# Performance work log

Measured on AMD Instinct MI355X. Metric: run time of the kernel, lower is better.

## Reference

```python
import jax, jax.numpy as jnp
import numpy as np
from jax import lax

SEQ_LEN, BATCH, POSE, H, PRED_LEN = 32, 32768, 34, 16, 15


def setup_inputs() -> dict:
    key = jax.random.key(0)
    ks = jax.random.split(key, 22)
    w = lambda k, s: (jax.random.normal(k, s, jnp.float32) * 0.1)
    return {
        "obs_s": jax.random.normal(ks[0], (SEQ_LEN, BATCH, POSE), jnp.float32),
        "enc_Wih": w(ks[1], (4 * H, POSE)), "enc_Whh": w(ks[2], (4 * H, H)),
        "enc_bih": w(ks[3], (4 * H,)), "enc_bhh": w(ks[4], (4 * H,)),
        "dec_Wih": w(ks[5], (4 * H, POSE)), "dec_Whh": w(ks[6], (4 * H, H)),
        "dec_bih": w(ks[7], (4 * H,)), "dec_bhh": w(ks[8], (4 * H,)),
        "cr_Wih": w(ks[9], (4 * H, POSE)), "cr_Whh": w(ks[10], (4 * H, H)),
        "cr_bih": w(ks[11], (4 * H,)), "cr_bhh": w(ks[12], (4 * H,)),
        "fc_W": w(ks[13], (POSE, H)), "fc_b": w(ks[14], (POSE,)),
        "fcc_W": w(ks[15], (2, H)), "fcc_b": w(ks[16], (2,)),
        "mlp_W": w(ks[17], (H, H)), "mlp_b": w(ks[18], (H,)),
        "emb_W": w(ks[19], (POSE, 2)), "emb_b": w(ks[20], (POSE,)),
        "pred_len": PRED_LEN,
    }


def _cell(x, h, c, Wih, Whh, bih, bhh):
    # torch LSTM gate order: i, f, g, o
    gates = x @ Wih.T + bih + h @ Whh.T + bhh  # [B, 4H]
    i, f, g, o = jnp.split(gates, 4, axis=-1)
    c = jax.nn.sigmoid(f) * c + jax.nn.sigmoid(i) * jnp.tanh(g)
    h = jax.nn.sigmoid(o) * jnp.tanh(c)
    return h, c


def reference(obs_s, enc_Wih, enc_Whh, enc_bih, enc_bhh,
              dec_Wih, dec_Whh, dec_bih, dec_bhh,
              cr_Wih, cr_Whh, cr_bih, cr_bhh,
              fc_W, fc_b, fcc_W, fcc_b, mlp_W, mlp_b, emb_W, emb_b,
              pred_len):
    batch = obs_s.shape[1]
    h0 = jnp.zeros((batch, H), obs_s.dtype)
    c0 = jnp.zeros((batch, H), obs_s.dtype)

    def enc_step(carry, x):
        h, c = _cell(x, *carry, enc_Wih, enc_Whh, enc_bih, enc_bhh)
        return (h, c), None

    (h, c), _ = lax.scan(enc_step, (h0, c0), obs_s)

    hc = h @ mlp_W.T + mlp_b           # crossing hidden init from encoder h
    cc = jnp.zeros_like(hc)
    last_s = obs_s[-1]                 # [B, POSE]
    last_cr = obs_s[-1]

    def dec_step(carry, _):
        h, c, hc, cc, last_s, last_cr = carry
        hc, cc = _cell(last_cr, hc, cc, cr_Wih, cr_Whh, cr_bih, cr_bhh)
        curr_cr = jax.nn.softmax(hc @ fcc_W.T + fcc_b, axis=-1)   # [B, 2]
        next_cr = curr_cr @ emb_W.T + emb_b                        # [B, POSE]
        h, c = _cell(last_s, h, c, dec_Wih, dec_Whh, dec_bih, dec_bhh)
        curr_s = h @ fc_W.T + fc_b                                 # [B, POSE]
        return (h, c, hc, cc, curr_s, next_cr), (curr_s, curr_cr)

    _, (pred_s, pred_crossing) = lax.scan(
        dec_step, (h, c, hc, cc, last_s, last_cr), None, length=pred_len)
    return pred_s, pred_crossing
```

## Files before the change

kernel.cpp:

```cpp
#include <hip/hip_runtime.h>
#include <cstddef>

#define SEQLEN 32
#define BATCH  32768
#define POSE   34
#define PREDL  15
#define LOG2E  1.4426950408889634f
#define K2E    2.8853901817779268f

typedef __attribute__((ext_vector_type(8))) short short8;
typedef __attribute__((ext_vector_type(4))) float f32x4;
typedef union { short8 s8; unsigned u[4]; } pk8;

#define MF(a,b,c) __builtin_amdgcn_mfma_f32_16x16x32_bf16(a,b,c,0,0,0)
#define EXP2(x)  __builtin_amdgcn_exp2f(x)
#define RCP(x)   __builtin_amdgcn_rcpf(x)

__device__ __forceinline__ unsigned short f2bf(float f){ __bf16 b=(__bf16)f; return __builtin_bit_cast(unsigned short,b); }
__device__ __forceinline__ unsigned f22bf(float lo,float hi){ return (unsigned)f2bf(lo) | ((unsigned)f2bf(hi)<<16); }
__device__ __forceinline__ short8 zero8(){ pk8 r; r.u[0]=0;r.u[1]=0;r.u[2]=0;r.u[3]=0; return r.s8; }
__device__ __forceinline__ float scGT(int gt){ return (gt==2)?K2E:LOG2E; }

__device__ __forceinline__ short8 g8s(const float* __restrict__ p, float s){
    pk8 r;
    r.u[0]=f22bf(p[0]*s,p[1]*s); r.u[1]=f22bf(p[2]*s,p[3]*s);
    r.u[2]=f22bf(p[4]*s,p[5]*s); r.u[3]=f22bf(p[6]*s,p[7]*s);
    return r.s8;
}

__device__ __forceinline__ void pw4v(const f32x4 (&ac)[4], f32x4 &cs,
                                     unsigned &hp0, unsigned &hp1){
    f32x4 A,C,B,O;
#pragma unroll
    for(int j=0;j<4;++j){
        A[j]=EXP2(-ac[0][j]); C[j]=EXP2(-ac[1][j]);
        B[j]=EXP2( ac[2][j]); O[j]=EXP2(-ac[3][j]);
    }
    const f32x4 one={1.f,1.f,1.f,1.f};
    f32x4 u=one+A, w=one+C, v=B+one, Bm=B-one;
    f32x4 t1=u*v;
    f32x4 num=cs*t1+Bm*w;
    f32x4 den=t1*w;
    f32x4 rd_,E,rh;
#pragma unroll
    for(int j=0;j<4;++j) rd_[j]=RCP(den[j]);
    f32x4 cn=num*rd_;
    cs=cn;
#pragma unroll
    for(int j=0;j<4;++j) E[j]=EXP2(K2E*cn[j]);
    f32x4 hd=(one+O)*(E+one);
#pragma unroll
    for(int j=0;j<4;++j) rh[j]=RCP(hd[j]);
    f32x4 hv=(E-one)*rh;
    hp0=f22bf(hv[0],hv[1]); hp1=f22bf(hv[2],hv[3]);
}

extern "C" __global__ void __launch_bounds__(256,2) lstm_enc(
    const float* __restrict__ obs_s,
    const float* __restrict__ eWih, const float* __restrict__ eWhh,
    const float* __restrict__ ebih, const float* __restrict__ ebhh,
    const float* __restrict__ mlpW, const float* __restrict__ mlpb,
    const float* __restrict__ dWih, const float* __restrict__ dWhh,
    const float* __restrict__ dbih, const float* __restrict__ dbhh,
    const float* __restrict__ cWih, const float* __restrict__ cWhh,
    const float* __restrict__ cbih, const float* __restrict__ cbhh,
    const float* __restrict__ fcW,  const float* __restrict__ fcb,
    const float* __restrict__ embW, const float* __restrict__ embb,
    float* __restrict__ wsBD, float* __restrict__ wsBC,
    unsigned short* __restrict__ wsDh, unsigned short* __restrict__ wsCh,
    unsigned short* __restrict__ wsCp, unsigned* __restrict__ hand)
{
    __shared__ unsigned xt4[4][4][320];

    if(blockIdx.x>=512){
        for(int idx=threadIdx.x; idx<1024; idx+=256){
            int R=idx>>4, k=idx&15;
            float s=scGT(R>>4);
            float vD=dWhh[R*16+k];
            for(int p=0;p<34;++p) vD=fmaf(dWih[R*34+p],fcW[p*16+k],vD);
            wsDh[idx]=f2bf(vD*s);
            wsCh[idx]=f2bf(cWhh[R*16+k]*s);
        }
        for(int idx=threadIdx.x; idx<128; idx+=256){
            int R=idx>>1, k=idx&1;
            float s=scGT(R>>4);
            float v=0.f;
            for(int p=0;p<34;++p) v=fmaf(cWih[R*34+p],embW[2*p+k],v);
            wsCp[idx]=f2bf(v*s);
        }
        for(int idx=threadIdx.x; idx<64; idx+=256){
            int R=idx;
            float s=scGT(R>>4);
            float vD=dbih[R]+dbhh[R], vC=cbih[R]+cbhh[R];
            for(int p=0;p<34;++p){ vD=fmaf(dWih[R*34+p],fcb[p],vD); vC=fmaf(cWih[R*34+p],embb[p],vC); }
            wsBD[idx]=vD*s; wsBC[idx]=vC*s;
        }
        return;
    }

    const int tid=threadIdx.x;
    const int l=tid&63;
    const int wv=tid>>6;
    const int lo=l&15, g=l>>4;
    const int pb=blockIdx.x*64 + wv*16;
    unsigned* XT=&xt4[wv][0][0];

    unsigned pofs[5]; int wofs[5];
#pragma unroll
    for(int it=0; it<5; ++it){
        int i2=l+64*it;
        int r=i2/17, w=i2-r*17;
        pofs[it]=(unsigned)((pb+r)*17+w);
        wofs[it]=r*20+w;
    }

    short8 wEx[4], wEhT[4]; f32x4 biasE[4];
#pragma unroll
    for(int gt=0;gt<4;++gt){
        float s=scGT(gt);
        int R=gt*16+lo;
        wEx[gt]=g8s(&eWih[R*34+8*g], s);
        pk8 r2;
        r2.u[0]=f22bf(eWhh[R*16+4*g]*s,   eWhh[R*16+4*g+1]*s);
        r2.u[1]=f22bf(eWhh[R*16+4*g+2]*s, eWhh[R*16+4*g+3]*s);
        r2.u[2]=(g==0)? f22bf(eWih[R*34+32]*s, eWih[R*34+33]*s) : 0u;
        r2.u[3]=0u;
        wEhT[gt]=r2.s8;
        float4 ba=*(const float4*)&ebih[gt*16+4*g];
        float4 bb=*(const float4*)&ebhh[gt*16+4*g];
        biasE[gt]=f32x4{(ba.x+bb.x)*s,(ba.y+bb.y)*s,(ba.z+bb.z)*s,(ba.w+bb.w)*s};
    }

    f32x4 cS={0.f,0.f,0.f,0.f};
    unsigned hp0=0u, hp1=0u;

    float2 RA[4][5];
    auto ldblk=[&](int t0){
#pragma unroll
        for(int s=0;s<4;++s){
            const float2* base=(const float2*)obs_s + (size_t)(t0+s)*(BATCH*17);
#pragma unroll
            for(int it=0;it<5;++it)
                if(it<4 || l<16) RA[s][it]=base[pofs[it]];
        }
    };
    auto wrblk=[&](){
#pragma unroll
        for(int s=0;s<4;++s)
#pragma unroll
            for(int it=0;it<5;++it)
                if(it<4 || l<16) XT[s*320+wofs[it]]=f22bf(RA[s][it].x,RA[s][it].y);
    };

    ldblk(0);
#pragma unroll 1
    for(int kb=0;kb<8;++kb){
        wrblk();
        if(kb+1<8) ldblk(4*(kb+1));
        short8 bx[4]; unsigned tw[4];
#pragma unroll
        for(int s=0;s<4;++s){
            bx[s]=*(const short8*)&XT[s*320+lo*20+4*g];
            tw[s]=XT[s*320+lo*20+16];
        }
        f32x4 cx[4][4];
#pragma unroll
        for(int s=0;s<4;++s)
#pragma unroll
            for(int gt=0;gt<4;++gt)
                cx[s][gt]=MF(wEx[gt],bx[s],biasE[gt]);
#pragma unroll
        for(int s=0;s<4;++s){
            pk8 bh; bh.u[0]=hp0; bh.u[1]=hp1; bh.u[2]=(g==0)?tw[s]:0u; bh.u[3]=0u;
            f32x4 acc[4];
#pragma unroll
            for(int gt=0;gt<4;++gt) acc[gt]=MF(wEhT[gt],bh.s8,cx[s][gt]);
            pw4v(acc,cS,hp0,hp1);
        }
    }

    unsigned hcp0,hcp1;
    {
        pk8 r;
        r.u[0]=f22bf(mlpW[lo*16+4*g],   mlpW[lo*16+4*g+1]);
        r.u[1]=f22bf(mlpW[lo*16+4*g+2], mlpW[lo*16+4*g+3]);
        r.u[2]=0u; r.u[3]=0u;
        f32x4 mb=*(const f32x4*)&mlpb[4*g];
        pk8 bh; bh.u[0]=hp0; bh.u[1]=hp1; bh.u[2]=0u; bh.u[3]=0u;
        f32x4 o=MF(r.s8,bh.s8,mb);
        hcp0=f22bf(o[0],o[1]); hcp1=f22bf(o[2],o[3]);
    }

    unsigned* Hw = hand + ((size_t)(blockIdx.x*4+wv)*64 + l)*8;
    Hw[0]=hp0; Hw[1]=hp1; Hw[2]=hcp0; Hw[3]=hcp1;
    *(f32x4*)(Hw+4)=cS;
}

extern "C" __global__ void __launch_bounds__(256,2) lstm_dec(
    const float* __restrict__ obs_s,
    const float* __restrict__ dWih, const float* __restrict__ dWhh,
    const float* __restrict__ dbih, const float* __restrict__ dbhh,
    const float* __restrict__ cWih, const float* __restrict__ cWhh,
    const float* __restrict__ cbih, const float* __restrict__ cbhh,
    const float* __restrict__ fcW,  const float* __restrict__ fcb,
    const float* __restrict__ fccW, const float* __restrict__ fccb,
    const float* __restrict__ wsBD, const float* __restrict__ wsBC,
    const unsigned short* __restrict__ wsDh, const unsigned short* __restrict__ wsCh,
    const unsigned short* __restrict__ wsCp, const unsigned* __restrict__ hand,
    float* __restrict__ out_s, float* __restrict__ out_cr)
{
    const int tid=threadIdx.x;
    const int l=tid&63;
    const int wv=tid>>6;
    const int lo=l&15, g=l>>4;
    const int grp=blockIdx.x*2+(wv>>1);
    const int role=__builtin_amdgcn_readfirstlane(wv&1);
    const int pb=grp*16;

    const unsigned* H = hand + ((size_t)grp*64 + l)*8;
    unsigned h0w=H[0], h1w=H[1], hc0w=H[2], hc1w=H[3];
    f32x4 csIn=*(const f32x4*)(H+4);

    const float* px=obs_s+((size_t)(SEQLEN-1)*BATCH+pb+lo)*POSE;
    short8 fbQ;
    {
        const float2* p2=(const float2*)(px+8*g);
        float2 q0=p2[0],q1=p2[1],q2=p2[2],q3=p2[3];
        pk8 r;
        r.u[0]=f22bf(q0.x,q0.y); r.u[1]=f22bf(q1.x,q1.y);
        r.u[2]=f22bf(q2.x,q2.y); r.u[3]=f22bf(q3.x,q3.y);
        fbQ=r.s8;
    }
    unsigned ftQ=f22bf(px[32],px[33]);

    if(role==0){
        f32x4 cS=csIn;
        unsigned hp0=h0w, hp1=h1w;
        f32x4 aD[4];
        {
#pragma unroll
            for(int gt=0;gt<4;++gt){
                float s=scGT(gt);
                int R=gt*16+lo;
                short8 d1=g8s(&dWih[R*34+8*g], s);
                pk8 d2;
                d2.u[0]=f22bf(dWhh[R*16+4*g]*s,   dWhh[R*16+4*g+1]*s);
                d2.u[1]=f22bf(dWhh[R*16+4*g+2]*s, dWhh[R*16+4*g+3]*s);
                d2.u[2]=(g==0)? f22bf(dWih[R*34+32]*s, dWih[R*34+33]*s) : 0u;
                d2.u[3]=0u;
                float4 da=*(const float4*)&dbih[gt*16+4*g];
                float4 db=*(const float4*)&dbhh[gt*16+4*g];
                f32x4 bd0={(da.x+db.x)*s,(da.y+db.y)*s,(da.z+db.z)*s,(da.w+db.w)*s};
                pk8 bhd; bhd.u[0]=hp0; bhd.u[1]=hp1; bhd.u[2]=(g==0)?ftQ:0u; bhd.u[3]=0u;
                f32x4 dx=MF(d1,fbQ,bd0);
                aD[gt]=MF(d2.s8,bhd.s8,dx);
            }
        }
        short8 wF[3]; f32x4 fcbF[3];
#pragma unroll
        for(int nt=0;nt<3;++nt){
            int np=nt*16+lo;
            if(np<POSE){
                pk8 r;
                r.u[0]=f22bf(fcW[np*16+4*g],   fcW[np*16+4*g+1]);
                r.u[1]=f22bf(fcW[np*16+4*g+2], fcW[np*16+4*g+3]);
                r.u[2]=0u; r.u[3]=0u;
                wF[nt]=r.s8;
            } else wF[nt]=zero8();
#pragma unroll
            for(int j=0;j<4;++j){
                int row=nt*16+4*g+j;
                fcbF[nt][j]=(row<POSE)? fcb[row] : 0.f;
            }
        }
        short8 wDh[4]; f32x4 biasD[4];
#pragma unroll
        for(int gt=0;gt<4;++gt){
            int R=gt*16+lo;
            uint2 qd=*(const uint2*)&wsDh[R*16+4*g];
            pk8 rd; rd.u[0]=qd.x; rd.u[1]=qd.y; rd.u[2]=0u; rd.u[3]=0u;
            wDh[gt]=rd.s8;
            biasD[gt]=*(const f32x4*)&wsBD[gt*16+4*g];
        }
#pragma unroll 1
        for(int s=0;s<PREDL;++s){
            pw4v(aD,cS,hp0,hp1);
            pk8 bh; bh.u[0]=hp0; bh.u[1]=hp1; bh.u[2]=0u; bh.u[3]=0u;
            f32x4 o0=MF(wF[0],bh.s8,fcbF[0]);
            f32x4 o1=MF(wF[1],bh.s8,fcbF[1]);
            f32x4 o2=MF(wF[2],bh.s8,fcbF[2]);
            float* po = out_s + ((size_t)s*BATCH + pb + lo)*POSE;
            *(float2*)(po+4*g)     =make_float2(o0[0],o0[1]);
            *(float2*)(po+4*g+2)   =make_float2(o0[2],o0[3]);
            *(float2*)(po+16+4*g)  =make_float2(o1[0],o1[1]);
            *(float2*)(po+16+4*g+2)=make_float2(o1[2],o1[3]);
            if(g==0) *(float2*)(po+32)=make_float2(o2[0],o2[1]);
            if(s+1<PREDL){
#pragma unroll
                for(int gt=0;gt<4;++gt) aD[gt]=MF(wDh[gt],bh.s8,biasD[gt]);
            }
        }
    } else {
        f32x4 cC={0.f,0.f,0.f,0.f};
        unsigned hcp0=hc0w, hcp1=hc1w, pp=0u;
        f32x4 aC[4];
        {
#pragma unroll
            for(int gt=0;gt<4;++gt){
                float s=scGT(gt);
                int R=gt*16+lo;
                short8 a1=g8s(&cWih[R*34+8*g], s);
                pk8 a2;
                a2.u[0]=f22bf(cWhh[R*16+4*g]*s,   cWhh[R*16+4*g+1]*s);
                a2.u[1]=f22bf(cWhh[R*16+4*g+2]*s, cWhh[R*16+4*g+3]*s);
                a2.u[2]=(g==0)? f22bf(cWih[R*34+32]*s, cWih[R*34+33]*s) : 0u;
                a2.u[3]=0u;
                float4 ba=*(const float4*)&cbih[gt*16+4*g];
                float4 bb=*(const float4*)&cbhh[gt*16+4*g];
                f32x4 bc0={(ba.x+bb.x)*s,(ba.y+bb.y)*s,(ba.z+bb.z)*s,(ba.w+bb.w)*s};
                pk8 bhc; bhc.u[0]=hcp0; bhc.u[1]=hcp1; bhc.u[2]=(g==0)?ftQ:0u; bhc.u[3]=0u;
                f32x4 cx=MF(a1,fbQ,bc0);
                aC[gt]=MF(a2.s8,bhc.s8,cx);
            }
        }
        short8 wFC; f32x4 fccC;
        if(lo<2){
            pk8 r;
            r.u[0]=f22bf(fccW[lo*16+4*g],   fccW[lo*16+4*g+1]);
            r.u[1]=f22bf(fccW[lo*16+4*g+2], fccW[lo*16+4*g+3]);
            r.u[2]=0u; r.u[3]=0u; wFC=r.s8;
        } else wFC=zero8();
        fccC=(g==0)? f32x4{fccb[0],fccb[1],0.f,0.f} : f32x4{0.f,0.f,0.f,0.f};
        short8 wCA[4]; f32x4 biasC[4];
#pragma unroll
        for(int gt=0;gt<4;++gt){
            int R=gt*16+lo;
            uint2 qc=*(const uint2*)&wsCh[R*16+4*g];
            pk8 rc; rc.u[0]=qc.x; rc.u[1]=qc.y;
            rc.u[2]=(g==0)? *(const unsigned*)&wsCp[R*2] : 0u; rc.u[3]=0u;
            wCA[gt]=rc.s8;
            biasC[gt]=*(const f32x4*)&wsBC[gt*16+4*g];
        }
#pragma unroll 1
        for(int s=0;s<PREDL;++s){
            pw4v(aC,cC,hcp0,hcp1);
            pk8 bhc2; bhc2.u[0]=hcp0; bhc2.u[1]=hcp1; bhc2.u[2]=0u; bhc2.u[3]=0u;
            f32x4 zz=MF(wFC,bhc2.s8,fccC);
            float z0=zz[0], z1=zz[1];
            float mx=fmaxf(z0,z1);
            float e0=EXP2(LOG2E*(z0-mx)), e1=EXP2(LOG2E*(z1-mx));
            float rs=RCP(e0+e1);
            float p0=e0*rs, p1=e1*rs;
            unsigned ppn=f22bf(p0,p1);
            if(g==0)
                ((float2*)out_cr)[(size_t)s*BATCH+pb+lo]=make_float2(p0,p1);
            pp=(unsigned)__shfl((int)ppn, lo, 64);
            if(s+1<PREDL){
                pk8 bc; bc.u[0]=hcp0; bc.u[1]=hcp1; bc.u[2]=(g==0)?pp:0u; bc.u[3]=0u;
#pragma unroll
                for(int gt=0;gt<4;++gt) aC[gt]=MF(wCA[gt],bc.s8,biasC[gt]);
            }
        }
    }
}

extern "C" void kernel_launch(void* const* d_in, const int* in_sizes, int n_in,
                              void* d_out, int out_size, void* d_ws, size_t ws_size,
                              hipStream_t stream)
{
    const float* obs  = (const float*)d_in[0];
    const float* eWih = (const float*)d_in[1];
    const float* eWhh = (const float*)d_in[2];
    const float* ebih = (const float*)d_in[3];
    const float* ebhh = (const float*)d_in[4];
    const float* dWih = (const float*)d_in[5];
    const float* dWhh = (const float*)d_in[6];
    const float* dbih = (const float*)d_in[7];
    const float* dbhh = (const float*)d_in[8];
    const float* cWih = (const float*)d_in[9];
    const float* cWhh = (const float*)d_in[10];
    const float* cbih = (const float*)d_in[11];
    const float* cbhh = (const float*)d_in[12];
    const float* fcW  = (const float*)d_in[13];
    const float* fcb  = (const float*)d_in[14];
    const float* fccW = (const float*)d_in[15];
    const float* fccb = (const float*)d_in[16];
    const float* mlpW = (const float*)d_in[17];
    const float* mlpb = (const float*)d_in[18];
    const float* embW = (const float*)d_in[19];
    const float* embb = (const float*)d_in[20];

    float* out_s  = (float*)d_out;
    float* out_cr = out_s + (size_t)PREDL*BATCH*POSE;

    float* wsBD = (float*)d_ws;
    float* wsBC = wsBD + 64;
    unsigned short* wsDh = (unsigned short*)(wsBC+64);
    unsigned short* wsCh = wsDh + 1024;
    unsigned short* wsCp = wsCh + 1024;
    unsigned* hand = (unsigned*)((char*)d_ws + 8192);

    hipLaunchKernelGGL(lstm_enc, dim3(513), dim3(256), 0, stream,
                       obs, eWih, eWhh, ebih, ebhh, mlpW, mlpb,
                       dWih, dWhh, dbih, dbhh, cWih, cWhh, cbih, cbhh,
                       fcW, fcb, embW, embb,
                       wsBD, wsBC, wsDh, wsCh, wsCp, hand);
    hipLaunchKernelGGL(lstm_dec, dim3(BATCH/32), dim3(256), 0, stream,
                       obs, dWih, dWhh, dbih, dbhh, cWih, cWhh, cbih, cbhh,
                       fcW, fcb, fccW, fccb,
                       wsBD, wsBC, wsDh, wsCh, wsCp, hand,
                       out_s, out_cr);
}
```

Before: 65.45 us.

## Halve encoder rows per wave to double grid size and fold bias into MFMA

Each encoder wave now handles 8 batch rows instead of 16. The 16-wide MFMA N dimension is filled by duplicating those rows (lq=lo&7), which doubles the grid to 1024 working blocks to raise parallelism across the recurrent chain. Timesteps are staged two at a time instead of four, and the bias moves into the K-padding slot of the recurrent MFMA through a constant-one column, freeing the bias registers. The handoff layout becomes indexed per batch row, and the decoder reads it the same way. The cost is duplicate MFMA work and twice as many waves each doing the full 32-step serial loop.

Measured after the change: 76.68 us. 1.17x slower.

```diff
diff --git a/kernel.cpp b/kernel.cpp
--- a/kernel.cpp
+++ b/kernel.cpp
@@ -70,9 +70,9 @@
     unsigned short* __restrict__ wsDh, unsigned short* __restrict__ wsCh,
     unsigned short* __restrict__ wsCp, unsigned* __restrict__ hand)
 {
-    __shared__ unsigned xt4[4][4][320];
-
-    if(blockIdx.x>=512){
+    __shared__ unsigned xt2[4][2][160];
+
+    if(blockIdx.x>=1024){
         for(int idx=threadIdx.x; idx<1024; idx+=256){
             int R=idx>>4, k=idx&15;
             float s=scGT(R>>4);
@@ -102,19 +102,21 @@
     const int l=tid&63;
     const int wv=tid>>6;
     const int lo=l&15, g=l>>4;
-    const int pb=blockIdx.x*64 + wv*16;
-    unsigned* XT=&xt4[wv][0][0];
-
-    unsigned pofs[5]; int wofs[5];
-#pragma unroll
-    for(int it=0; it<5; ++it){
+    const int lq=lo&7;
+    const int pb=blockIdx.x*32 + wv*8;
+    unsigned* XT=&xt2[wv][0][0];
+
+    unsigned pofs[3]; int wofs[3];
+#pragma unroll
+    for(int it=0; it<3; ++it){
         int i2=l+64*it;
-        int r=i2/17, w=i2-r*17;
+        int r=(i2/17)&7, w=i2-(i2/17)*17;
         pofs[it]=(unsigned)((pb+r)*17+w);
         wofs[it]=r*20+w;
     }
 
-    short8 wEx[4], wEhT[4]; f32x4 biasE[4];
+    short8 wEx[4], wEhT[4];
+    const f32x4 z4={0.f,0.f,0.f,0.f};
 #pragma unroll
     for(int gt=0;gt<4;++gt){
         float s=scGT(gt);
@@ -124,57 +126,58 @@
         r2.u[0]=f22bf(eWhh[R*16+4*g]*s,   eWhh[R*16+4*g+1]*s);
         r2.u[1]=f22bf(eWhh[R*16+4*g+2]*s, eWhh[R*16+4*g+3]*s);
         r2.u[2]=(g==0)? f22bf(eWih[R*34+32]*s, eWih[R*34+33]*s) : 0u;
-        r2.u[3]=0u;
+        r2.u[3]=(g==0)? f22bf((ebih[R]+ebhh[R])*s, 0.f) : 0u;
         wEhT[gt]=r2.s8;
-        float4 ba=*(const float4*)&ebih[gt*16+4*g];
-        float4 bb=*(const float4*)&ebhh[gt*16+4*g];
-        biasE[gt]=f32x4{(ba.x+bb.x)*s,(ba.y+bb.y)*s,(ba.z+bb.z)*s,(ba.w+bb.w)*s};
-    }
+    }
+    const unsigned oneSlot=(g==0)? 0x00003F80u : 0u;
 
     f32x4 cS={0.f,0.f,0.f,0.f};
     unsigned hp0=0u, hp1=0u;
 
-    float2 RA[4][5];
+    float2 RA[2][3];
     auto ldblk=[&](int t0){
 #pragma unroll
-        for(int s=0;s<4;++s){
-            const float2* base=(const float2*)obs_s + (size_t)(t0+s)*(BATCH*17);
-#pragma unroll
-            for(int it=0;it<5;++it)
-                if(it<4 || l<16) RA[s][it]=base[pofs[it]];
+        for(int s2=0;s2<2;++s2){
+            const float2* base=(const float2*)obs_s + (size_t)(t0+s2)*(BATCH*17);
+#pragma unroll
+            for(int it=0;it<3;++it)
+                if(it<2 || l<8) RA[s2][it]=base[pofs[it]];
         }
     };
     auto wrblk=[&](){
 #pragma unroll
-        for(int s=0;s<4;++s)
-#pragma unroll
-            for(int it=0;it<5;++it)
-                if(it<4 || l<16) XT[s*320+wofs[it]]=f22bf(RA[s][it].x,RA[s][it].y);
+        for(int s2=0;s2<2;++s2)
+#pragma unroll
+            for(int it=0;it<3;++it)
+                if(it<2 || l<8) XT[s2*160+wofs[it]]=f22bf(RA[s2][it].x,RA[s2][it].y);
     };
 
+    short8 fbQ=zero8(); unsigned ftQ=0u;
     ldblk(0);
 #pragma unroll 1
-    for(int kb=0;kb<8;++kb){
+    for(int kb=0;kb<16;++kb){
         wrblk();
-        if(kb+1<8) ldblk(4*(kb+1));
-        short8 bx[4]; unsigned tw[4];
-#pragma unroll
-        for(int s=0;s<4;++s){
-            bx[s]=*(const short8*)&XT[s*320+lo*20+4*g];
-            tw[s]=XT[s*320+lo*20+16];
-        }
-        f32x4 cx[4][4];
-#pragma unroll
-        for(int s=0;s<4;++s)
+        if(kb+1<16) ldblk(2*(kb+1));
+        short8 bx[2]; unsigned tw[2];
+#pragma unroll
+        for(int s2=0;s2<2;++s2){
+            bx[s2]=*(const short8*)&XT[s2*160+lq*20+4*g];
+            tw[s2]=XT[s2*160+lq*20+16];
+        }
+        f32x4 cx[2][4];
+#pragma unroll
+        for(int s2=0;s2<2;++s2)
 #pragma unroll
             for(int gt=0;gt<4;++gt)
-                cx[s][gt]=MF(wEx[gt],bx[s],biasE[gt]);
-#pragma unroll
-        for(int s=0;s<4;++s){
-            pk8 bh; bh.u[0]=hp0; bh.u[1]=hp1; bh.u[2]=(g==0)?tw[s]:0u; bh.u[3]=0u;
+                cx[s2][gt]=MF(wEx[gt],bx[s2],z4);
+        fbQ=bx[1]; ftQ=tw[1];
+#pragma unroll
+        for(int s2=0;s2<2;++s2){
+            pk8 bh; bh.u[0]=hp0; bh.u[1]=hp1;
+            bh.u[2]=(g==0)?tw[s2]:0u; bh.u[3]=oneSlot;
             f32x4 acc[4];
 #pragma unroll
-            for(int gt=0;gt<4;++gt) acc[gt]=MF(wEhT[gt],bh.s8,cx[s][gt]);
+            for(int gt=0;gt<4;++gt) acc[gt]=MF(wEhT[gt],bh.s8,cx[s2][gt]);
             pw4v(acc,cS,hp0,hp1);
         }
     }
@@ -191,9 +194,11 @@
         hcp0=f22bf(o[0],o[1]); hcp1=f22bf(o[2],o[3]);
     }
 
-    unsigned* Hw = hand + ((size_t)(blockIdx.x*4+wv)*64 + l)*8;
-    Hw[0]=hp0; Hw[1]=hp1; Hw[2]=hcp0; Hw[3]=hcp1;
-    *(f32x4*)(Hw+4)=cS;
+    if(lo<8){
+        unsigned* Hw = hand + (((size_t)(pb+lq))*4 + g)*8;
+        Hw[0]=hp0; Hw[1]=hp1; Hw[2]=hcp0; Hw[3]=hcp1;
+        *(f32x4*)(Hw+4)=cS;
+    }
 }
 
 extern "C" __global__ void __launch_bounds__(256,2) lstm_dec(
@@ -217,7 +222,7 @@
     const int role=__builtin_amdgcn_readfirstlane(wv&1);
     const int pb=grp*16;
 
-    const unsigned* H = hand + ((size_t)grp*64 + l)*8;
+    const unsigned* H = hand + (((size_t)(pb+lo))*4 + g)*8;
     unsigned h0w=H[0], h1w=H[1], hc0w=H[2], hc1w=H[3];
     f32x4 csIn=*(const f32x4*)(H+4);
 
@@ -400,7 +405,7 @@
     unsigned short* wsCp = wsCh + 1024;
     unsigned* hand = (unsigned*)((char*)d_ws + 8192);
 
-    hipLaunchKernelGGL(lstm_enc, dim3(513), dim3(256), 0, stream,
+    hipLaunchKernelGGL(lstm_enc, dim3(1025), dim3(256), 0, stream,
                        obs, eWih, eWhh, ebih, ebhh, mlpW, mlpb,
                        dWih, dWhh, dbih, dbhh, cWih, cWhh, cbih, cbhh,
                        fcW, fcb, embW, embb,
```
